# Kernel optimization log

Hardware: AMD Instinct MI355X
Metric: run time of the kernel (lower is better)

## Reference

```python
import jax, jax.numpy as jnp
import numpy as np

HEAD = 16
H_DIM = 64  # dims // head
ROT = 32    # h_dim // 2


def setup_inputs() -> dict:
    key = jax.random.key(0)
    k1, k2, k3, k4 = jax.random.split(key, 4)
    B, S, D = 8, 4096, 1024
    x = jax.random.normal(k1, (B, S, D), dtype=jnp.float32)
    thetas = jax.random.normal(k2, (ROT,), dtype=jnp.float32) * 0.1
    theta_scale = jnp.ones((1,), dtype=jnp.float32)
    # near-orthogonal matrix, as r_matrix is initialized to eye
    r_matrix = jnp.eye(H_DIM, dtype=jnp.float32) + 0.01 * jax.random.normal(k3, (H_DIM, H_DIM), dtype=jnp.float32)
    base = 10000.0
    inv_freq = (1.0 / base ** (jnp.arange(0, H_DIM, 2, dtype=jnp.float32) / H_DIM)).astype(jnp.float32)
    # rotation plane index pairs (i, j) with i != j, as produced by update_pairs()
    i_idx = jax.random.randint(k4, (ROT,), 0, H_DIM)
    off = jax.random.randint(jax.random.fold_in(k4, 1), (ROT,), 1, H_DIM)
    j_idx = (i_idx + off) % H_DIM
    pairs = jnp.stack([i_idx, j_idx], axis=1).astype(jnp.int32)
    return {"x": x, "thetas": thetas, "theta_scale": theta_scale,
            "r_matrix": r_matrix, "inv_freq": inv_freq, "pairs": pairs}


def _blended_rotation(xf, pairs, thetas_scaled):
    """Apply rot sequential blended Givens rotations to xf [N, H_DIM].

    B = (G + H + R)/3 with G == R the Givens rotation in plane (i,j) and
    H = I - 2 v v^T (v = [cos, sin] in plane (i,j), ||v|| = 1).
    x @ B only changes columns i and j; all other columns pass through
    since (2*x_k + x_k)/3 = x_k. This is mathematically identical to the
    original dense h_dim x h_dim matmul per step.
    """
    def step(xc, inp):
        i, j, th = inp["i"], inp["j"], inp["th"]
        c, s = jnp.cos(th), jnp.sin(th)
        xi = jnp.take(xc, i, axis=1)
        xj = jnp.take(xc, j, axis=1)
        gi = xi * c + xj * s        # (x @ G) column i; also equals x . v
        gj = -xi * s + xj * c       # (x @ G) column j
        ni = (2.0 * gi + xi - 2.0 * gi * c) / 3.0
        nj = (2.0 * gj + xj - 2.0 * gi * s) / 3.0
        xc = xc.at[:, i].set(ni)
        xc = xc.at[:, j].set(nj)
        return xc, None
    xf, _ = jax.lax.scan(step, xf, {"i": pairs[:, 0], "j": pairs[:, 1], "th": thetas_scaled})
    return xf


def reference(x, thetas, theta_scale, r_matrix, inv_freq, pairs):
    B, S, D = x.shape
    xf = x.reshape(-1, H_DIM)                       # [B*S*head, h_dim]
    # adjusted_rot = int(round(rot_scale * rot)) == rot for rot_scale = 1
    xf = _blended_rotation(xf, pairs, thetas * theta_scale[0])
    xf = xf @ r_matrix
    xr = xf.reshape(B, S, HEAD, H_DIM)
    # RoPE-style sin/cos mix (note: concatenated halves, not interleaved)
    pos = jnp.arange(S, dtype=x.dtype)
    sinu = pos[:, None] * inv_freq[None, :]          # [S, h_dim/2]
    sin = jnp.sin(sinu)[None, :, None, :]
    cos = jnp.cos(sinu)[None, :, None, :]
    x1, x2 = xr[..., ::2], xr[..., 1::2]
    out = jnp.concatenate([x1 * cos - x2 * sin, x1 * sin + x2 * cos], axis=-1)
    return out.reshape(B, S, D)
```

## Files before the change

### kernel.cpp

```cpp
#include <hip/hip_runtime.h>

#define HEADS 16
#define HD 64
#define ROT 32
#define SEQ 4096
#define BROWS 256

typedef float sv16 __attribute__((ext_vector_type(16)));

__global__ __launch_bounds__(256) void build_W_kernel(
    const float* __restrict__ thetas,
    const float* __restrict__ theta_scale,
    const float* __restrict__ r_matrix,
    const int* __restrict__ pairs,
    float* __restrict__ Wp)
{
    __shared__ float M[64][65];
    __shared__ float Rl[64][65];
    __shared__ int   ip[32], jp[32];
    __shared__ float cs[32], sn[32];
    const int tid = threadIdx.x;

    if (tid < 32) {
        const int i = pairs[2 * tid + 0];
        const int j = pairs[2 * tid + 1];
        float s, c;
        sincosf(thetas[tid] * theta_scale[0], &s, &c);
        ip[tid] = i; jp[tid] = j; cs[tid] = c; sn[tid] = s;
    }
    #pragma unroll
    for (int it = 0; it < 16; ++it) {
        const int f = it * 256 + tid;
        Rl[f >> 6][f & 63] = r_matrix[f];
    }
    if (tid < 64) {
        #pragma unroll
        for (int k = 0; k < 64; ++k) M[tid][k] = (k == tid) ? 1.0f : 0.0f;
    }
    __syncthreads();

    if (tid < 64) {
        const int t = tid;
        #pragma unroll 1
        for (int r = 0; r < ROT; ++r) {
            const int i = ip[r];
            const int j = jp[r];
            const float c = cs[r];
            const float s = sn[r];
            const float xi = M[t][i];
            const float xj = M[t][j];
            const float gi =  xi * c + xj * s;
            const float gj = -xi * s + xj * c;
            const float ni = (2.0f * gi + xi - 2.0f * gi * c) / 3.0f;
            const float nj = (2.0f * gj + xj - 2.0f * gi * s) / 3.0f;
            M[t][i] = ni;
            M[t][j] = nj;
        }
    }
    __syncthreads();

    const int n = tid & 63;
    const int kq = tid >> 6;
    const int cn = (n < 32) ? (2 * n) : (2 * (n - 32) + 1);
    #pragma unroll 1
    for (int kk = 0; kk < 16; ++kk) {
        const int k = kq * 16 + kk;
        float acc = 0.0f;
        #pragma unroll
        for (int j = 0; j < 64; ++j) acc = fmaf(M[k][j], Rl[j][cn], acc);
        Wp[k * 64 + n] = acc;
    }
}

#define PREF(C0, C1, OA, OB) asm volatile(                       \
    "s_load_dwordx16 %0, %2, " #OA "\n\t"                         \
    "s_load_dwordx16 %1, %2, " #OB                                \
    : "=&s"(C0), "=&s"(C1) : "s"(wq))

#define WAITW(C0, C1) asm volatile("s_waitcnt lgkmcnt(0)" : "+s"(C0), "+s"(C1))

#define FMA32(C0, C1, M, H) do { const float xm_ = xkf[M];        \
    _Pragma("unroll")                                             \
    for (int i_ = 0; i_ < 16; ++i_) {                             \
        acc[(H)*32 + i_]      = fmaf(xm_, (C0)[i_], acc[(H)*32 + i_]);      \
        acc[(H)*32 + 16 + i_] = fmaf(xm_, (C1)[i_], acc[(H)*32 + 16 + i_]); \
    } } while (0)

__global__ __launch_bounds__(256, 5) void fused_main(
    const float* __restrict__ x,
    const float* __restrict__ Wp,
    const float* __restrict__ inv_freq,
    float* __restrict__ out)
{
    __shared__ float tc[16 * 33];
    __shared__ float tsn[16 * 33];

    const int tid = threadIdx.x;
    const int blk = blockIdx.x;
    const long long row = (long long)blk * BROWS + tid;
    const float4* __restrict__ xp4 = (const float4*)(x + row * HD);
    float4* __restrict__ op4 = (float4*)(out + row * HD);

    {
        const int s0 = (blk & (SEQ / 16 - 1)) * 16;
        #pragma unroll
        for (int u = 0; u < 2; ++u) {
            const int e = tid * 2 + u;
            const int sl = e >> 5;
            const int f = e & 31;
            const float ang = (float)(s0 + sl) * inv_freq[f];
            float s_, c_;
            sincosf(ang, &s_, &c_);
            tc[sl * 33 + f] = c_;
            tsn[sl * 33 + f] = s_;
        }
    }
    __syncthreads();

    float acc[64];
    #pragma unroll
    for (int nn = 0; nn < 64; ++nn) acc[nn] = 0.0f;

    #pragma unroll 1
    for (int q = 0; q < 4; ++q) {
        float xkf[16];
        {
            const float4 t0 = xp4[q * 4 + 0];
            const float4 t1 = xp4[q * 4 + 1];
            const float4 t2 = xp4[q * 4 + 2];
            const float4 t3 = xp4[q * 4 + 3];
            xkf[0]=t0.x;  xkf[1]=t0.y;  xkf[2]=t0.z;  xkf[3]=t0.w;
            xkf[4]=t1.x;  xkf[5]=t1.y;  xkf[6]=t1.z;  xkf[7]=t1.w;
            xkf[8]=t2.x;  xkf[9]=t2.y;  xkf[10]=t2.z; xkf[11]=t2.w;
            xkf[12]=t3.x; xkf[13]=t3.y; xkf[14]=t3.z; xkf[15]=t3.w;
        }
        const float* wq = Wp + q * 1024;
        sv16 A0, A1, B0, B1;

        PREF(A0, A1, 0, 64);            WAITW(A0, A1);
        PREF(B0, B1, 128, 192);   FMA32(A0, A1, 0, 0);  WAITW(B0, B1);
        PREF(A0, A1, 256, 320);   FMA32(B0, B1, 0, 1);  WAITW(A0, A1);
        PREF(B0, B1, 384, 448);   FMA32(A0, A1, 1, 0);  WAITW(B0, B1);
        PREF(A0, A1, 512, 576);   FMA32(B0, B1, 1, 1);  WAITW(A0, A1);
        PREF(B0, B1, 640, 704);   FMA32(A0, A1, 2, 0);  WAITW(B0, B1);
        PREF(A0, A1, 768, 832);   FMA32(B0, B1, 2, 1);  WAITW(A0, A1);
        PREF(B0, B1, 896, 960);   FMA32(A0, A1, 3, 0);  WAITW(B0, B1);
        PREF(A0, A1, 1024, 1088); FMA32(B0, B1, 3, 1);  WAITW(A0, A1);
        PREF(B0, B1, 1152, 1216); FMA32(A0, A1, 4, 0);  WAITW(B0, B1);
        PREF(A0, A1, 1280, 1344); FMA32(B0, B1, 4, 1);  WAITW(A0, A1);
        PREF(B0, B1, 1408, 1472); FMA32(A0, A1, 5, 0);  WAITW(B0, B1);
        PREF(A0, A1, 1536, 1600); FMA32(B0, B1, 5, 1);  WAITW(A0, A1);
        PREF(B0, B1, 1664, 1728); FMA32(A0, A1, 6, 0);  WAITW(B0, B1);
        PREF(A0, A1, 1792, 1856); FMA32(B0, B1, 6, 1);  WAITW(A0, A1);
        PREF(B0, B1, 1920, 1984); FMA32(A0, A1, 7, 0);  WAITW(B0, B1);
        PREF(A0, A1, 2048, 2112); FMA32(B0, B1, 7, 1);  WAITW(A0, A1);
        PREF(B0, B1, 2176, 2240); FMA32(A0, A1, 8, 0);  WAITW(B0, B1);
        PREF(A0, A1, 2304, 2368); FMA32(B0, B1, 8, 1);  WAITW(A0, A1);
        PREF(B0, B1, 2432, 2496); FMA32(A0, A1, 9, 0);  WAITW(B0, B1);
        PREF(A0, A1, 2560, 2624); FMA32(B0, B1, 9, 1);  WAITW(A0, A1);
        PREF(B0, B1, 2688, 2752); FMA32(A0, A1, 10, 0); WAITW(B0, B1);
        PREF(A0, A1, 2816, 2880); FMA32(B0, B1, 10, 1); WAITW(A0, A1);
        PREF(B0, B1, 2944, 3008); FMA32(A0, A1, 11, 0); WAITW(B0, B1);
        PREF(A0, A1, 3072, 3136); FMA32(B0, B1, 11, 1); WAITW(A0, A1);
        PREF(B0, B1, 3200, 3264); FMA32(A0, A1, 12, 0); WAITW(B0, B1);
        PREF(A0, A1, 3328, 3392); FMA32(B0, B1, 12, 1); WAITW(A0, A1);
        PREF(B0, B1, 3456, 3520); FMA32(A0, A1, 13, 0); WAITW(B0, B1);
        PREF(A0, A1, 3584, 3648); FMA32(B0, B1, 13, 1); WAITW(A0, A1);
        PREF(B0, B1, 3712, 3776); FMA32(A0, A1, 14, 0); WAITW(B0, B1);
        PREF(A0, A1, 3840, 3904); FMA32(B0, B1, 14, 1); WAITW(A0, A1);
        PREF(B0, B1, 3968, 4032); FMA32(A0, A1, 15, 0); WAITW(B0, B1);
        FMA32(B0, B1, 15, 1);
    }

    {
        const int sl = tid >> 4;
        #pragma unroll
        for (int n = 0; n < 32; ++n) {
            const float c = tc[sl * 33 + n];
            const float s = tsn[sl * 33 + n];
            const float a = acc[n];
            const float b = acc[32 + n];
            acc[n]      = a * c - b * s;
            acc[32 + n] = a * s + b * c;
        }
    }

    #pragma unroll
    for (int c = 0; c < 16; ++c) {
        op4[c] = make_float4(acc[4 * c + 0], acc[4 * c + 1],
                             acc[4 * c + 2], acc[4 * c + 3]);
    }
}

extern "C" void kernel_launch(void* const* d_in, const int* in_sizes, int n_in,
                              void* d_out, int out_size, void* d_ws, size_t ws_size,
                              hipStream_t stream) {
    const float* x   = (const float*)d_in[0];
    const float* th  = (const float*)d_in[1];
    const float* sc  = (const float*)d_in[2];
    const float* R   = (const float*)d_in[3];
    const float* ivf = (const float*)d_in[4];
    const int*   pr  = (const int*)d_in[5];
    float* W = (float*)d_ws;

    build_W_kernel<<<1, 256, 0, stream>>>(th, sc, R, pr, W);

    const int rows = out_size / HD;
    const int blocks = rows / BROWS;
    fused_main<<<blocks, 256, 0, stream>>>(x, W, ivf, (float*)d_out);
}
```

Baseline: 347.0 us.

## Stage x loads and output stores through padded LDS for coalesced global access

Before, each thread read and wrote its own 256-byte row with strided float4 accesses. Now the block loads x cooperatively, in two halves, into a padded shared-memory tile so that global reads are coalesced across threads. Each thread then reads its row from LDS. Output is written back the same way, in two halves through LDS. This adds LDS traffic and several barriers, and lowers the occupancy hint from 5 to 4 blocks because of the roughly 33 KB shared tile.

```diff
diff --git a/kernel.cpp b/kernel.cpp
--- a/kernel.cpp
+++ b/kernel.cpp
@@ -5,6 +5,7 @@
 #define ROT 32
 #define SEQ 4096
 #define BROWS 256
+#define PADW 33
 
 typedef float sv16 __attribute__((ext_vector_type(16)));
 
@@ -72,34 +73,75 @@
     }
 }
 
-#define PREF(C0, C1, OA, OB) asm volatile(                       \
+#define PREF(C0, C1, OA, OB) asm volatile(                        \
     "s_load_dwordx16 %0, %2, " #OA "\n\t"                         \
     "s_load_dwordx16 %1, %2, " #OB                                \
     : "=&s"(C0), "=&s"(C1) : "s"(wq))
 
 #define WAITW(C0, C1) asm volatile("s_waitcnt lgkmcnt(0)" : "+s"(C0), "+s"(C1))
 
-#define FMA32(C0, C1, M, H) do { const float xm_ = xkf[M];        \
-    _Pragma("unroll")                                             \
-    for (int i_ = 0; i_ < 16; ++i_) {                             \
+#define FMA32(C0, C1, M, H) do { const float xm_ = xkf[M];                  \
+    _Pragma("unroll")                                                       \
+    for (int i_ = 0; i_ < 16; ++i_) {                                       \
         acc[(H)*32 + i_]      = fmaf(xm_, (C0)[i_], acc[(H)*32 + i_]);      \
         acc[(H)*32 + 16 + i_] = fmaf(xm_, (C1)[i_], acc[(H)*32 + 16 + i_]); \
     } } while (0)
 
-__global__ __launch_bounds__(256, 5) void fused_main(
+__device__ __forceinline__ void quarter_ladder(const float* __restrict__ wq,
+                                               const float (&xkf)[16],
+                                               float (&acc)[64])
+{
+    sv16 A0, A1, B0, B1;
+    PREF(A0, A1, 0, 64);            WAITW(A0, A1);
+    PREF(B0, B1, 128, 192);   FMA32(A0, A1, 0, 0);  WAITW(B0, B1);
+    PREF(A0, A1, 256, 320);   FMA32(B0, B1, 0, 1);  WAITW(A0, A1);
+    PREF(B0, B1, 384, 448);   FMA32(A0, A1, 1, 0);  WAITW(B0, B1);
+    PREF(A0, A1, 512, 576);   FMA32(B0, B1, 1, 1);  WAITW(A0, A1);
+    PREF(B0, B1, 640, 704);   FMA32(A0, A1, 2, 0);  WAITW(B0, B1);
+    PREF(A0, A1, 768, 832);   FMA32(B0, B1, 2, 1);  WAITW(A0, A1);
+    PREF(B0, B1, 896, 960);   FMA32(A0, A1, 3, 0);  WAITW(B0, B1);
+    PREF(A0, A1, 1024, 1088); FMA32(B0, B1, 3, 1);  WAITW(A0, A1);
+    PREF(B0, B1, 1152, 1216); FMA32(A0, A1, 4, 0);  WAITW(B0, B1);
+    PREF(A0, A1, 1280, 1344); FMA32(B0, B1, 4, 1);  WAITW(A0, A1);
+    PREF(B0, B1, 1408, 1472); FMA32(A0, A1, 5, 0);  WAITW(B0, B1);
+    PREF(A0, A1, 1536, 1600); FMA32(B0, B1, 5, 1);  WAITW(A0, A1);
+    PREF(B0, B1, 1664, 1728); FMA32(A0, A1, 6, 0);  WAITW(B0, B1);
+    PREF(A0, A1, 1792, 1856); FMA32(B0, B1, 6, 1);  WAITW(A0, A1);
+    PREF(B0, B1, 1920, 1984); FMA32(A0, A1, 7, 0);  WAITW(B0, B1);
+    PREF(A0, A1, 2048, 2112); FMA32(B0, B1, 7, 1);  WAITW(A0, A1);
+    PREF(B0, B1, 2176, 2240); FMA32(A0, A1, 8, 0);  WAITW(B0, B1);
+    PREF(A0, A1, 2304, 2368); FMA32(B0, B1, 8, 1);  WAITW(A0, A1);
+    PREF(B0, B1, 2432, 2496); FMA32(A0, A1, 9, 0);  WAITW(B0, B1);
+    PREF(A0, A1, 2560, 2624); FMA32(B0, B1, 9, 1);  WAITW(A0, A1);
+    PREF(B0, B1, 2688, 2752); FMA32(A0, A1, 10, 0); WAITW(B0, B1);
+    PREF(A0, A1, 2816, 2880); FMA32(B0, B1, 10, 1); WAITW(A0, A1);
+    PREF(B0, B1, 2944, 3008); FMA32(A0, A1, 11, 0); WAITW(B0, B1);
+    PREF(A0, A1, 3072, 3136); FMA32(B0, B1, 11, 1); WAITW(A0, A1);
+    PREF(B0, B1, 3200, 3264); FMA32(A0, A1, 12, 0); WAITW(B0, B1);
+    PREF(A0, A1, 3328, 3392); FMA32(B0, B1, 12, 1); WAITW(A0, A1);
+    PREF(B0, B1, 3456, 3520); FMA32(A0, A1, 13, 0); WAITW(B0, B1);
+    PREF(A0, A1, 3584, 3648); FMA32(B0, B1, 13, 1); WAITW(A0, A1);
+    PREF(B0, B1, 3712, 3776); FMA32(A0, A1, 14, 0); WAITW(B0, B1);
+    PREF(A0, A1, 3840, 3904); FMA32(B0, B1, 14, 1); WAITW(A0, A1);
+    PREF(B0, B1, 3968, 4032); FMA32(A0, A1, 15, 0); WAITW(B0, B1);
+    FMA32(B0, B1, 15, 1);
+}
+
+__global__ __launch_bounds__(256, 4) void fused_main(
     const float* __restrict__ x,
     const float* __restrict__ Wp,
     const float* __restrict__ inv_freq,
     float* __restrict__ out)
 {
+    __shared__ float xs[BROWS * PADW];
     __shared__ float tc[16 * 33];
     __shared__ float tsn[16 * 33];
 
     const int tid = threadIdx.x;
     const int blk = blockIdx.x;
-    const long long row = (long long)blk * BROWS + tid;
-    const float4* __restrict__ xp4 = (const float4*)(x + row * HD);
-    float4* __restrict__ op4 = (float4*)(out + row * HD);
+    const long long base4 = (long long)blk * (BROWS * HD / 4);
+    const float4* __restrict__ xv = (const float4*)x + base4;
+    float4* __restrict__ ov = (float4*)out + base4;
 
     {
         const int s0 = (blk & (SEQ / 16 - 1)) * 16;
@@ -115,61 +157,33 @@
             tsn[sl * 33 + f] = s_;
         }
     }
-    __syncthreads();
 
     float acc[64];
     #pragma unroll
     for (int nn = 0; nn < 64; ++nn) acc[nn] = 0.0f;
 
     #pragma unroll 1
-    for (int q = 0; q < 4; ++q) {
-        float xkf[16];
-        {
-            const float4 t0 = xp4[q * 4 + 0];
-            const float4 t1 = xp4[q * 4 + 1];
-            const float4 t2 = xp4[q * 4 + 2];
-            const float4 t3 = xp4[q * 4 + 3];
-            xkf[0]=t0.x;  xkf[1]=t0.y;  xkf[2]=t0.z;  xkf[3]=t0.w;
-            xkf[4]=t1.x;  xkf[5]=t1.y;  xkf[6]=t1.z;  xkf[7]=t1.w;
-            xkf[8]=t2.x;  xkf[9]=t2.y;  xkf[10]=t2.z; xkf[11]=t2.w;
-            xkf[12]=t3.x; xkf[13]=t3.y; xkf[14]=t3.z; xkf[15]=t3.w;
-        }
-        const float* wq = Wp + q * 1024;
-        sv16 A0, A1, B0, B1;
-
-        PREF(A0, A1, 0, 64);            WAITW(A0, A1);
-        PREF(B0, B1, 128, 192);   FMA32(A0, A1, 0, 0);  WAITW(B0, B1);
-        PREF(A0, A1, 256, 320);   FMA32(B0, B1, 0, 1);  WAITW(A0, A1);
-        PREF(B0, B1, 384, 448);   FMA32(A0, A1, 1, 0);  WAITW(B0, B1);
-        PREF(A0, A1, 512, 576);   FMA32(B0, B1, 1, 1);  WAITW(A0, A1);
-        PREF(B0, B1, 640, 704);   FMA32(A0, A1, 2, 0);  WAITW(B0, B1);
-        PREF(A0, A1, 768, 832);   FMA32(B0, B1, 2, 1);  WAITW(A0, A1);
-        PREF(B0, B1, 896, 960);   FMA32(A0, A1, 3, 0);  WAITW(B0, B1);
-        PREF(A0, A1, 1024, 1088); FMA32(B0, B1, 3, 1);  WAITW(A0, A1);
-        PREF(B0, B1, 1152, 1216); FMA32(A0, A1, 4, 0);  WAITW(B0, B1);
-        PREF(A0, A1, 1280, 1344); FMA32(B0, B1, 4, 1);  WAITW(A0, A1);
-        PREF(B0, B1, 1408, 1472); FMA32(A0, A1, 5, 0);  WAITW(B0, B1);
-        PREF(A0, A1, 1536, 1600); FMA32(B0, B1, 5, 1);  WAITW(A0, A1);
-        PREF(B0, B1, 1664, 1728); FMA32(A0, A1, 6, 0);  WAITW(B0, B1);
-        PREF(A0, A1, 1792, 1856); FMA32(B0, B1, 6, 1);  WAITW(A0, A1);
-        PREF(B0, B1, 1920, 1984); FMA32(A0, A1, 7, 0);  WAITW(B0, B1);
-        PREF(A0, A1, 2048, 2112); FMA32(B0, B1, 7, 1);  WAITW(A0, A1);
-        PREF(B0, B1, 2176, 2240); FMA32(A0, A1, 8, 0);  WAITW(B0, B1);
-        PREF(A0, A1, 2304, 2368); FMA32(B0, B1, 8, 1);  WAITW(A0, A1);
-        PREF(B0, B1, 2432, 2496); FMA32(A0, A1, 9, 0);  WAITW(B0, B1);
-        PREF(A0, A1, 2560, 2624); FMA32(B0, B1, 9, 1);  WAITW(A0, A1);
-        PREF(B0, B1, 2688, 2752); FMA32(A0, A1, 10, 0); WAITW(B0, B1);
-        PREF(A0, A1, 2816, 2880); FMA32(B0, B1, 10, 1); WAITW(A0, A1);
-        PREF(B0, B1, 2944, 3008); FMA32(A0, A1, 11, 0); WAITW(B0, B1);
-        PREF(A0, A1, 3072, 3136); FMA32(B0, B1, 11, 1); WAITW(A0, A1);
-        PREF(B0, B1, 3200, 3264); FMA32(A0, A1, 12, 0); WAITW(B0, B1);
-        PREF(A0, A1, 3328, 3392); FMA32(B0, B1, 12, 1); WAITW(A0, A1);
-        PREF(B0, B1, 3456, 3520); FMA32(A0, A1, 13, 0); WAITW(B0, B1);
-        PREF(A0, A1, 3584, 3648); FMA32(B0, B1, 13, 1); WAITW(A0, A1);
-        PREF(B0, B1, 3712, 3776); FMA32(A0, A1, 14, 0); WAITW(B0, B1);
-        PREF(A0, A1, 3840, 3904); FMA32(B0, B1, 14, 1); WAITW(A0, A1);
-        PREF(B0, B1, 3968, 4032); FMA32(A0, A1, 15, 0); WAITW(B0, B1);
-        FMA32(B0, B1, 15, 1);
+    for (int half = 0; half < 2; ++half) {
+        __syncthreads();
+        #pragma unroll
+        for (int it = 0; it < 8; ++it) {
+            const int f = it * 256 + tid;
+            const int row = f >> 3;
+            const int c4 = f & 7;
+            const float4 v = xv[row * 16 + half * 8 + c4];
+            float* p = &xs[row * PADW + c4 * 4];
+            p[0] = v.x; p[1] = v.y; p[2] = v.z; p[3] = v.w;
+        }
+        __syncthreads();
+
+        const float* xrow = &xs[tid * PADW];
+        #pragma unroll 1
+        for (int kc = 0; kc < 2; ++kc) {
+            float xkf[16];
+            #pragma unroll
+            for (int m = 0; m < 16; ++m) xkf[m] = xrow[kc * 16 + m];
+            quarter_ladder(Wp + (half * 32 + kc * 16) * 64, xkf, acc);
+        }
     }
 
     {
@@ -185,10 +199,32 @@
         }
     }
 
-    #pragma unroll
-    for (int c = 0; c < 16; ++c) {
-        op4[c] = make_float4(acc[4 * c + 0], acc[4 * c + 1],
-                             acc[4 * c + 2], acc[4 * c + 3]);
+    {
+        float* prow = &xs[tid * PADW];
+        __syncthreads();
+        #pragma unroll
+        for (int n = 0; n < 32; ++n) prow[n] = acc[n];
+        __syncthreads();
+        #pragma unroll
+        for (int it = 0; it < 8; ++it) {
+            const int f = it * 256 + tid;
+            const int row = f >> 3;
+            const int c4 = f & 7;
+            const float* p = &xs[row * PADW + c4 * 4];
+            ov[row * 16 + c4] = make_float4(p[0], p[1], p[2], p[3]);
+        }
+        __syncthreads();
+        #pragma unroll
+        for (int n = 0; n < 32; ++n) prow[n] = acc[32 + n];
+        __syncthreads();
+        #pragma unroll
+        for (int it = 0; it < 8; ++it) {
+            const int f = it * 256 + tid;
+            const int row = f >> 3;
+            const int c4 = f & 7;
+            const float* p = &xs[row * PADW + c4 * 4];
+            ov[row * 16 + 8 + c4] = make_float4(p[0], p[1], p[2], p[3]);
+        }
     }
 }
 
```

New measurement: 290.7 us. 16.2% less time.
